# Kernel tuning notes

Hardware: AMD Instinct MI355X
Metric: run time of the kernel (lower is better)

The kernel has to match this reference:

```python
import jax, jax.numpy as jnp
import numpy as np

N = 80000
E = 1280000
EPS = 1e-5

def _lrelu(x):
    return jax.nn.leaky_relu(x, 0.01)

def _bn(h):
    # training-mode BatchNorm1d with batch size 1: stats over the node dim; affine is identity at init
    return (h - h.mean(0)) / jnp.sqrt(h.var(0) + EPS)

def _ln(h, g, b):
    m = h.mean(-1, keepdims=True)
    v = h.var(-1, keepdims=True)
    return (h - m) / jnp.sqrt(v + EPS) * g + b

def _gcn(h, w, b, src, dst, n):
    # PyG GCNConv: add self loops, symmetric deg^-1/2 normalization, aggregate at target
    hw = h @ w.T
    loop = jnp.arange(n, dtype=src.dtype)
    s = jnp.concatenate([src, loop])
    d = jnp.concatenate([dst, loop])
    deg = jax.ops.segment_sum(jnp.ones(d.shape, hw.dtype), d, num_segments=n)
    dinv = jnp.where(deg > 0, 1.0 / jnp.sqrt(deg), 0.0)
    msg = hw[s] * (dinv[s] * dinv[d])[:, None]  # [E+N, C]
    return jax.ops.segment_sum(msg, d, num_segments=n) + b

def _tnet(x, c1w, c1b, c2w, c2b, c3w, c3b, f1w, f1b, f2w, f2b, f3w, f3b):
    h = jax.nn.relu(x @ c1w.T + c1b)          # [N,64]  (source skips bn1)
    h = jax.nn.relu(_bn(h @ c2w.T + c2b))     # [N,128]
    h = jax.nn.relu(_bn(h @ c3w.T + c3b))     # [N,1024]
    g = h.max(0)                              # global max pool -> [1024]
    g = jax.nn.relu(g @ f1w.T + f1b)
    g = jax.nn.relu(g @ f2w.T + f2b)
    iden = jnp.array([1.0, 0.0, 0.0, 0.0, 1.0, 0.0, 0.0, 0.0, 1.0], x.dtype)
    g = g @ f3w.T + f3b + iden
    return g.reshape(3, 3)

def _forward(edge_index, x, tnet_c1_w, tnet_c1_b, tnet_c2_w, tnet_c2_b, tnet_c3_w, tnet_c3_b, tnet_fc1_w, tnet_fc1_b, tnet_fc2_w, tnet_fc2_b, tnet_fc3_w, tnet_fc3_b, conv1_w, conv1_b, g1_li_w, g1_li_b, g1_gcn_w, g1_gcn_b, g1_ln_g, g1_ln_b, conv2_w, conv2_b, g2_li_w, g2_li_b, g2_gcn_w, g2_gcn_b, g2_ln_g, g2_ln_b, conv3_w, conv3_b, out_w, out_b):
    src, dst = edge_index[0], edge_index[1]
    n = x.shape[0]
    T = _tnet(x, tnet_c1_w, tnet_c1_b, tnet_c2_w, tnet_c2_b, tnet_c3_w, tnet_c3_b, tnet_fc1_w, tnet_fc1_b, tnet_fc2_w, tnet_fc2_b, tnet_fc3_w, tnet_fc3_b)
    h0 = x @ T                                  # [N,3] spatial transform
    xg = _lrelu(h0 @ conv1_w.T + conv1_b)       # [N,64] (conv1d k=1 == per-node linear)
    # Gcn_Attention 1
    nf = _lrelu(xg @ g1_li_w.T + g1_li_b)
    nf2 = _lrelu(_gcn(nf, g1_gcn_w, g1_gcn_b, src, dst, n))
    h = _ln(jnp.concatenate([nf, nf2], 1), g1_ln_g, g1_ln_b)   # [N,128]
    h = _lrelu(h @ conv2_w.T + conv2_b)
    # Gcn_Attention 2
    nf = _lrelu(h @ g2_li_w.T + g2_li_b)
    nf2 = _lrelu(_gcn(nf, g2_gcn_w, g2_gcn_b, src, dst, n))
    h = _ln(jnp.concatenate([nf, nf2], 1), g2_ln_g, g2_ln_b)   # [N,256]
    h = jnp.concatenate([h, xg], 1)                            # [N,320]
    h = _lrelu(h @ conv3_w.T + conv3_b)                        # [N,256]
    pooled = h.mean(0)                                         # global mean pool (single graph)
    feat = jnp.concatenate([jnp.broadcast_to(pooled, (n, pooled.shape[0])), xg], 1)  # [N,320]
    return feat @ out_w.T + out_b                              # [N,4]

def setup_inputs():
    ki = iter(jax.random.split(jax.random.key(0), 32))
    def W(shape):
        return jax.random.normal(next(ki), shape, jnp.float32) * (1.0 / float(np.sqrt(shape[-1])))
    z = lambda n: jnp.zeros((n,), jnp.float32)
    o = lambda n: jnp.ones((n,), jnp.float32)
    inp = {}
    inp['x'] = jax.random.normal(next(ki), (N, 3), jnp.float32)
    inp['edge_index'] = jax.random.randint(next(ki), (2, E), 0, N, dtype=jnp.int32)
    inp['tnet_c1_w'] = W((64, 3)); inp['tnet_c1_b'] = z(64)
    inp['tnet_c2_w'] = W((128, 64)); inp['tnet_c2_b'] = z(128)
    inp['tnet_c3_w'] = W((1024, 128)); inp['tnet_c3_b'] = z(1024)
    inp['tnet_fc1_w'] = W((512, 1024)); inp['tnet_fc1_b'] = z(512)
    inp['tnet_fc2_w'] = W((256, 512)); inp['tnet_fc2_b'] = z(256)
    inp['tnet_fc3_w'] = W((9, 256)); inp['tnet_fc3_b'] = z(9)
    inp['conv1_w'] = W((64, 3)); inp['conv1_b'] = z(64)
    inp['g1_li_w'] = W((64, 64)); inp['g1_li_b'] = z(64)
    inp['g1_gcn_w'] = W((64, 64)); inp['g1_gcn_b'] = z(64)
    inp['g1_ln_g'] = o(128); inp['g1_ln_b'] = z(128)
    inp['conv2_w'] = W((128, 128)); inp['conv2_b'] = z(128)
    inp['g2_li_w'] = W((128, 128)); inp['g2_li_b'] = z(128)
    inp['g2_gcn_w'] = W((128, 128)); inp['g2_gcn_b'] = z(128)
    inp['g2_ln_g'] = o(256); inp['g2_ln_b'] = z(256)
    inp['conv3_w'] = W((256, 320)); inp['conv3_b'] = z(256)
    inp['out_w'] = W((4, 320)); inp['out_b'] = z(4)
    return inp

def reference(x, edge_index, tnet_c1_w, tnet_c1_b, tnet_c2_w, tnet_c2_b, tnet_c3_w, tnet_c3_b, tnet_fc1_w, tnet_fc1_b, tnet_fc2_w, tnet_fc2_b, tnet_fc3_w, tnet_fc3_b, conv1_w, conv1_b, g1_li_w, g1_li_b, g1_gcn_w, g1_gcn_b, g1_ln_g, g1_ln_b, conv2_w, conv2_b, g2_li_w, g2_li_b, g2_gcn_w, g2_gcn_b, g2_ln_g, g2_ln_b, conv3_w, conv3_b, out_w, out_b):
    return _forward(edge_index, x, tnet_c1_w, tnet_c1_b, tnet_c2_w, tnet_c2_b, tnet_c3_w, tnet_c3_b, tnet_fc1_w, tnet_fc1_b, tnet_fc2_w, tnet_fc2_b, tnet_fc3_w, tnet_fc3_b, conv1_w, conv1_b, g1_li_w, g1_li_b, g1_gcn_w, g1_gcn_b, g1_ln_g, g1_ln_b, conv2_w, conv2_b, g2_li_w, g2_li_b, g2_gcn_w, g2_gcn_b, g2_ln_g, g2_ln_b, conv3_w, conv3_b, out_w, out_b)
```

## Files before the change

### kernel.cpp

```cpp
#include <hip/hip_runtime.h>
#include <cstddef>

#define EPSV 1e-5f

typedef __attribute__((ext_vector_type(8))) short frag8;
typedef __attribute__((ext_vector_type(4))) float f32x4;

__device__ __forceinline__ float lrelu01(float v) { return v > 0.f ? v : 0.01f * v; }
__device__ __forceinline__ void atomAddF(float* p, float v) { unsafeAtomicAdd(p, v); }
__device__ __forceinline__ unsigned fkey(float f) {
    unsigned u = __float_as_uint(f);
    return (u & 0x80000000u) ? ~u : (u | 0x80000000u);
}
__device__ __forceinline__ unsigned short f2b(float f) {
    unsigned u = __float_as_uint(f);
    unsigned r = u + 0x7fffu + ((u >> 16) & 1u);
    return (unsigned short)(r >> 16);
}
__device__ __forceinline__ float b2f(unsigned short h) {
    return __uint_as_float(((unsigned)h) << 16);
}
__device__ __forceinline__ float blo(unsigned u) { return __uint_as_float(u << 16); }
__device__ __forceinline__ float bhi(unsigned u) { return __uint_as_float(u & 0xffff0000u); }

static inline unsigned cdivu(unsigned a, unsigned b) { return (a + b - 1) / b; }

__device__ __forceinline__ void gbar(unsigned* cnt, unsigned target) {
    __syncthreads();
    if (threadIdx.x == 0) {
        __threadfence();
        atomicAdd(cnt, 1u);
        while (atomicAdd(cnt, 0u) < target) { }
        __threadfence();
    }
    __syncthreads();
}


__device__ void degrank_body(int bid, const int* __restrict__ dst, int* __restrict__ deg,
                             int* __restrict__ rank, int E) {
    int e = bid * 256 + threadIdx.x;
    if (e < E) rank[e] = atomicAdd(&deg[dst[e]], 1);
}

__device__ void scan_local_body(int bid, const int* __restrict__ deg, int* __restrict__ startv,
                                int* __restrict__ bsum, float* __restrict__ dinv, int n) {
    __shared__ int t0[256];
    int tid = threadIdx.x;
    int i = bid * 256 + tid;
    int v = (i < n) ? deg[i] : 0;
    if (i < n) dinv[i] = rsqrtf((float)(v + 1));
    t0[tid] = v;
    __syncthreads();
    for (int o = 1; o < 256; o <<= 1) {
        int add = (tid >= o) ? t0[tid - o] : 0;
        __syncthreads();
        t0[tid] += add;
        __syncthreads();
    }
    if (i < n) startv[i] = t0[tid] - v;
    if (tid == 255) bsum[bid] = t0[255];
}

__device__ void scan_bsum_body(int* __restrict__ bsum, int nb) {
    __shared__ int t0[512];
    __shared__ int t1[512];
    int tid = threadIdx.x;
    int v0 = (tid < nb) ? bsum[tid] : 0;
    int v1 = (tid + 256 < nb) ? bsum[tid + 256] : 0;
    t0[tid] = v0; t0[tid + 256] = v1;
    __syncthreads();
    int* a = t0; int* b = t1;
    for (int o = 1; o < 512; o <<= 1) {
        b[tid]       = a[tid]       + ((tid >= o)       ? a[tid - o]       : 0);
        b[tid + 256] = a[tid + 256] + ((tid + 256 >= o) ? a[tid + 256 - o] : 0);
        __syncthreads();
        int* t = a; a = b; b = t;
    }
    if (tid < nb) bsum[tid] = a[tid] - v0;
    if (tid + 256 < nb) bsum[tid + 256] = a[tid + 256] - v1;
}

__device__ void fill_body(int bid, const int* __restrict__ src, const int* __restrict__ dst,
                          const int* __restrict__ rank, const int* __restrict__ startv,
                          const int* __restrict__ bsum, int* __restrict__ csr, int E) {
    int e = bid * 256 + threadIdx.x;
    if (e < E) {
        int d = dst[e];
        csr[startv[d] + bsum[d >> 8] + rank[e]] = src[e];
    }
}


__device__ void wconv_body(int bid, const float* __restrict__ s0, const float* __restrict__ s1,
                           const float* __restrict__ s2, const float* __restrict__ s3,
                           const float* __restrict__ s4, const float* __restrict__ s5,
                           const float* __restrict__ s6, const float* __restrict__ s7,
                           unsigned short* __restrict__ dst) {
    int t = bid * 256 + threadIdx.x;
    if (t >= 278528) return;
    const float* srcs[8] = {s0, s1, s2, s3, s4, s5, s6, s7};
    const int off[9] = {0, 8192, 139264, 143360, 147456, 163840, 180224, 196608, 278528};
    int seg = 0;
    while (t >= off[seg + 1]) ++seg;
    unsigned short v = f2b(srcs[seg][t - off[seg]]);
    if (seg == 1) {
        int li = t - 8192;
        int rch = li >> 7, k = li & 127;
        int cb = rch >> 7, r = rch & 127;
        int flat = ((r >> 4) * 4 + (k >> 5)) * 64 + ((k >> 3) & 3) * 16 + (r & 15);
        dst[8192 + cb * 16384 + flat * 8 + (k & 7)] = v;
    } else {
        dst[t] = v;
    }
}

__device__ void h1_body(int bid, const float* __restrict__ x, const float* __restrict__ w,
                        const float* __restrict__ b, unsigned short* __restrict__ h1, int n) {
    int node = bid * 256 + threadIdx.x;
    if (node >= n) return;
    float x0 = x[node * 3], x1 = x[node * 3 + 1], x2 = x[node * 3 + 2];
    unsigned short* o = h1 + (size_t)node * 64;
#pragma unroll
    for (int cp = 0; cp < 8; ++cp) {
        unsigned short tmp[8];
#pragma unroll
        for (int t = 0; t < 8; ++t) {
            int c = cp * 8 + t;
            float v = x0 * w[c * 3] + x1 * w[c * 3 + 1] + x2 * w[c * 3 + 2] + b[c];
            tmp[t] = f2b(fmaxf(v, 0.f));
        }
        *(float4*)(o + cp * 8) = *(float4*)tmp;
    }
}

__device__ void prebn_body(int bid, const float* __restrict__ z, const float* __restrict__ sum2,
                           const float* __restrict__ ss2, unsigned short* __restrict__ a3f,
                           int n16, float invn) {
    int t = bid * 256 + threadIdx.x;
    if (t >= n16) return;
    int row = t >> 4, cp = t & 15;
    int c = cp * 8;
    const float* src = z + (size_t)row * 128 + c;
    float4 v0 = *(const float4*)src;
    float4 v1 = *(const float4*)(src + 4);
    float vv[8] = {v0.x, v0.y, v0.z, v0.w, v1.x, v1.y, v1.z, v1.w};
    unsigned short o[8];
#pragma unroll
    for (int i = 0; i < 8; ++i) {
        float m = sum2[c + i] * invn;
        float var = ss2[c + i] * invn - m * m;
        o[i] = f2b(fmaxf((vv[i] - m) * rsqrtf(var + EPSV), 0.f));
    }
    int tile = row >> 7, r = row & 127;
    int flat = ((r >> 4) * 4 + (cp >> 2)) * 64 + (cp & 3) * 16 + (r & 15);
    *(float4*)(a3f + (size_t)tile * 16384 + flat * 8) = *(float4*)o;
}

enum { MF_BIAS = 1, MF_LRELU = 2, MF_DINV = 4, MF_STOREF = 8, MF_STOREB = 16,
       MF_STATS = 32, MF_COLSUM = 64 };

template <int BN, int MODE>
__device__ void mgemm_body(int bx, int by,
                           const unsigned short* __restrict__ A, int lda, int K,
                           const unsigned short* __restrict__ W,
                           const float* __restrict__ bias,
                           float* __restrict__ OutF, unsigned short* __restrict__ OutB, int ldo,
                           const float* __restrict__ dinv,
                           float* __restrict__ sum_o, float* __restrict__ ss_o,
                           unsigned* __restrict__ maxk_o) {
    constexpr int BM = 128;
    constexpr int LDT = 40;
    __shared__ unsigned short As[BM * LDT];
    __shared__ unsigned short Ws[BN * LDT];
    __shared__ float redS[2 * 128];
    __shared__ unsigned redM[128];

    const int tid = threadIdx.x;
    const int wid = tid >> 6, lane = tid & 63;
    const int quad = lane >> 4, lrow = lane & 15;
    const int bn0 = bx * BM;
    const int bc0 = by * BN;

    constexpr int NI = (BN == 128) ? 4 : 2;
    constexpr int NJ = 4;
    const int wm = (BN == 128) ? (wid & 1) * 64 : wid * 32;
    const int wn = (BN == 128) ? (wid >> 1) * 64 : 0;

    if (MODE & (MF_STATS | MF_COLSUM)) {
        for (int c = tid; c < BN; c += 256) {
            redS[c] = 0.f; redS[128 + c] = 0.f; redM[c] = 0u;
        }
    }

    f32x4 acc[NI][NJ] = {};

    for (int k0 = 0; k0 < K; k0 += 32) {
#pragma unroll
        for (int h = 0; h < 2; ++h) {
            int ch = tid + h * 256;
            int row = ch >> 2, cp = ch & 3;
            const unsigned short* src = A + (size_t)(bn0 + row) * lda + k0 + cp * 8;
            *(float4*)&As[row * LDT + cp * 8] = *(const float4*)src;
        }
#pragma unroll
        for (int h = 0; h < BN / 64; ++h) {
            int ch = tid + h * 256;
            int row = ch >> 2, cp = ch & 3;
            const unsigned short* src = W + (size_t)(bc0 + row) * K + k0 + cp * 8;
            *(float4*)&Ws[row * LDT + cp * 8] = *(const float4*)src;
        }
        __syncthreads();
        frag8 af[NI], bf[NJ];
#pragma unroll
        for (int i = 0; i < NI; ++i)
            af[i] = *(const frag8*)&As[(wm + i * 16 + lrow) * LDT + quad * 8];
#pragma unroll
        for (int j = 0; j < NJ; ++j)
            bf[j] = *(const frag8*)&Ws[(wn + j * 16 + lrow) * LDT + quad * 8];
#pragma unroll
        for (int i = 0; i < NI; ++i)
#pragma unroll
            for (int j = 0; j < NJ; ++j)
                acc[i][j] = __builtin_amdgcn_mfma_f32_16x16x32_bf16(af[i], bf[j], acc[i][j], 0, 0, 0);
        __syncthreads();
    }

#pragma unroll
    for (int j = 0; j < NJ; ++j) {
        const int col = bc0 + wn + j * 16 + lrow;
        float bv = (MODE & MF_BIAS) ? bias[col] : 0.f;
        float s = 0.f, q = 0.f, m = -3.4e38f;
#pragma unroll
        for (int i = 0; i < NI; ++i) {
            const int rowb = bn0 + wm + i * 16 + quad * 4;
#pragma unroll
            for (int r = 0; r < 4; ++r) {
                float t = acc[i][j][r] + bv;
                if (MODE & MF_LRELU) t = lrelu01(t);
                if (MODE & MF_DINV) t *= dinv[rowb + r];
                if (MODE & MF_STOREF) OutF[(size_t)(rowb + r) * ldo + col] = t;
                if (MODE & MF_STOREB) OutB[(size_t)(rowb + r) * ldo + col] = f2b(t);
                s += t; q += t * t; m = fmaxf(m, t);
            }
        }
        if (MODE & (MF_STATS | MF_COLSUM)) {
            s += __shfl_xor(s, 16); s += __shfl_xor(s, 32);
            if (MODE & MF_STATS) {
                q += __shfl_xor(q, 16); q += __shfl_xor(q, 32);
                m = fmaxf(m, __shfl_xor(m, 16)); m = fmaxf(m, __shfl_xor(m, 32));
            }
            if (quad == 0) {
                int lc = wn + j * 16 + lrow;
                atomicAdd(&redS[lc], s);
                if (MODE & MF_STATS) {
                    atomicAdd(&redS[128 + lc], q);
                    atomicMax(&redM[lc], fkey(m));
                }
            }
        }
    }
    if (MODE & (MF_STATS | MF_COLSUM)) {
        __syncthreads();
        for (int c = tid; c < BN; c += 256) {
            atomAddF(&sum_o[bc0 + c], redS[c]);
            if (MODE & MF_STATS) {
                atomAddF(&ss_o[bc0 + c], redS[128 + c]);
                atomicMax(&maxk_o[bc0 + c], redM[c]);
            }
        }
    }
}

template <int BN, int MODE, int SWAP>
__launch_bounds__(256)
__global__ void k_mgemm(const unsigned short* __restrict__ A, int lda, int K,
                        const unsigned short* __restrict__ W,
                        const float* __restrict__ bias,
                        float* __restrict__ OutF, unsigned short* __restrict__ OutB, int ldo,
                        const float* __restrict__ dinv,
                        float* __restrict__ sum_o, float* __restrict__ ss_o,
                        unsigned* __restrict__ maxk_o) {
    int bx = SWAP ? blockIdx.y : blockIdx.x;
    int by = SWAP ? blockIdx.x : blockIdx.y;
    mgemm_body<BN, MODE>(bx, by, A, lda, K, W, bias, OutF, OutB, ldo, dinv, sum_o, ss_o, maxk_o);
}

__device__ void z3_body(int bid,
                        const unsigned short* __restrict__ AF,
                        const unsigned short* __restrict__ WF,
                        const float* __restrict__ bias,
                        float* __restrict__ sum_o, float* __restrict__ ss_o,
                        unsigned* __restrict__ maxk_o, int ntiles) {
    const int tid = threadIdx.x;
    const int wid = tid >> 6, lane = tid & 63;
    const int quad = lane >> 4, lrow = lane & 15;

    int w = (bid & 7) * ntiles + (bid >> 3);
    const int tile = w >> 3;
    const int cb = w & 7;
    const unsigned short* At = AF + (size_t)tile * 16384;
    const unsigned short* Wt = WF + (size_t)cb * 16384;

    const int ar = (wid & 1) * 4;
    const int wc = (wid >> 1) * 4;
    f32x4 acc[4][4] = {};
#pragma unroll
    for (int kc = 0; kc < 4; ++kc) {
        frag8 af[4], bf[4];
#pragma unroll
        for (int i = 0; i < 4; ++i)
            af[i] = *(const frag8*)&At[(((ar + i) * 4 + kc) * 64 + lane) * 8];
#pragma unroll
        for (int j = 0; j < 4; ++j)
            bf[j] = *(const frag8*)&Wt[(((wc + j) * 4 + kc) * 64 + lane) * 8];
#pragma unroll
        for (int i = 0; i < 4; ++i)
#pragma unroll
            for (int j = 0; j < 4; ++j)
                acc[i][j] = __builtin_amdgcn_mfma_f32_16x16x32_bf16(af[i], bf[j], acc[i][j], 0, 0, 0);
    }

#pragma unroll
    for (int j = 0; j < 4; ++j) {
        int c = cb * 128 + (wc + j) * 16 + lrow;
        float bv = bias[c];
        float s = 0.f, q = 0.f, m = -3.4e38f;
#pragma unroll
        for (int i = 0; i < 4; ++i)
#pragma unroll
            for (int r = 0; r < 4; ++r) {
                float t = acc[i][j][r] + bv;
                s += t; q += t * t; m = fmaxf(m, t);
            }
        s += __shfl_xor(s, 16); s += __shfl_xor(s, 32);
        q += __shfl_xor(q, 16); q += __shfl_xor(q, 32);
        m = fmaxf(m, __shfl_xor(m, 16)); m = fmaxf(m, __shfl_xor(m, 32));
        if (quad == 0) {
            atomAddF(&sum_o[c], s);
            atomAddF(&ss_o[c], q);
            atomicMax(&maxk_o[c], fkey(m));
        }
    }
}


__launch_bounds__(256)
__global__ void FK1(const int* __restrict__ dst, int* __restrict__ deg, int* __restrict__ rank,
                    int E, int EB,
                    const float* s0, const float* s1, const float* s2, const float* s3,
                    const float* s4, const float* s5, const float* s6, const float* s7,
                    unsigned short* __restrict__ WB, int WCB,
                    const float* __restrict__ x, const float* __restrict__ c1w,
                    const float* __restrict__ c1b, unsigned short* __restrict__ B1, int n) {
    int b = blockIdx.x;
    if (b < EB) { degrank_body(b, dst, deg, rank, E); return; }
    b -= EB;
    if (b < WCB) { wconv_body(b, s0, s1, s2, s3, s4, s5, s6, s7, WB); return; }
    b -= WCB;
    h1_body(b, x, c1w, c1b, B1, n);
}

__launch_bounds__(256)
__global__ void FK2(const unsigned short* __restrict__ A, int lda, int K,
                    const unsigned short* __restrict__ W, const float* __restrict__ bias,
                    float* __restrict__ OutF, int ldo,
                    float* __restrict__ sum_o, float* __restrict__ ss_o,
                    unsigned* __restrict__ maxk_o, int GXz,
                    const int* __restrict__ deg, int* __restrict__ startv,
                    int* __restrict__ bsum, float* __restrict__ dinvv, int n) {
    if ((int)blockIdx.x < GXz)
        mgemm_body<128, (MF_BIAS | MF_STOREF | MF_STATS)>(
            blockIdx.x, 0, A, lda, K, W, bias, OutF, nullptr, ldo, nullptr, sum_o, ss_o, maxk_o);
    else
        scan_local_body(blockIdx.x - GXz, deg, startv, bsum, dinvv, n);
}

__launch_bounds__(256)
__global__ void FK3(const float* __restrict__ z, const float* __restrict__ sum2,
                    const float* __restrict__ ss2, unsigned short* __restrict__ a3f,
                    int n16, float invn, int PB, int* __restrict__ bsum, int nb) {
    if ((int)blockIdx.x < PB) prebn_body(blockIdx.x, z, sum2, ss2, a3f, n16, invn);
    else scan_bsum_body(bsum, nb);
}

__launch_bounds__(256)
__global__ void FK4(const unsigned short* __restrict__ AF, const unsigned short* __restrict__ WF,
                    const float* __restrict__ bias,
                    float* __restrict__ sum_o, float* __restrict__ ss_o,
                    unsigned* __restrict__ maxk_o, int ntiles, int NZ,
                    const int* __restrict__ src, const int* __restrict__ dst,
                    const int* __restrict__ rank, const int* __restrict__ startv,
                    const int* __restrict__ bsum, int* __restrict__ csr, int E) {
    if ((int)blockIdx.x < NZ) z3_body(blockIdx.x, AF, WF, bias, sum_o, ss_o, maxk_o, ntiles);
    else fill_body(blockIdx.x - NZ, src, dst, rank, startv, bsum, csr, E);
}

__launch_bounds__(256)
__global__ void k_tnet(const float* __restrict__ sum3, const float* __restrict__ ss3,
                       const unsigned* __restrict__ maxk,
                       const float* __restrict__ f1w, const float* __restrict__ f1b,
                       const float* __restrict__ f2w, const float* __restrict__ f2bias,
                       const float* __restrict__ f3w, const float* __restrict__ f3b,
                       float* __restrict__ a1, float* __restrict__ a2,
                       float* __restrict__ T9,
                       unsigned* __restrict__ cnt1, unsigned* __restrict__ cnt2, float invn) {
    __shared__ float g[1024];
    __shared__ float a1s[512];
    int tid = threadIdx.x;
    int bid = blockIdx.x;
    for (int c = tid; c < 1024; c += 256) {
        float m = sum3[c] * invn;
        float var = ss3[c] * invn - m * m;
        unsigned k = maxk[c];
        unsigned u = (k & 0x80000000u) ? (k & 0x7FFFFFFFu) : ~k;
        g[c] = fmaxf((__uint_as_float(u) - m) * rsqrtf(var + EPSV), 0.f);
    }
    __syncthreads();
    {
        int row = bid * 64 + (tid >> 2);
        int part = tid & 3;
        const float* w = f1w + (size_t)row * 1024 + part * 256;
        const float* gg = g + part * 256;
        float s = 0.f;
#pragma unroll 4
        for (int k = 0; k < 256; k += 4) {
            float4 wv = *(const float4*)(w + k);
            s = fmaf(wv.x, gg[k], s);
            s = fmaf(wv.y, gg[k + 1], s);
            s = fmaf(wv.z, gg[k + 2], s);
            s = fmaf(wv.w, gg[k + 3], s);
        }
        s += __shfl_xor(s, 1); s += __shfl_xor(s, 2);
        if (part == 0) a1[row] = fmaxf(s + f1b[row], 0.f);
    }
    gbar(cnt1, 8);
    a1s[tid] = a1[tid];
    a1s[tid + 256] = a1[tid + 256];
    __syncthreads();
    {
        int row = bid * 32 + (tid >> 3);
        int part = tid & 7;
        const float* w = f2w + (size_t)row * 512 + part * 64;
        const float* aa = a1s + part * 64;
        float s = 0.f;
#pragma unroll 4
        for (int k = 0; k < 64; k += 4) {
            float4 wv = *(const float4*)(w + k);
            s = fmaf(wv.x, aa[k], s);
            s = fmaf(wv.y, aa[k + 1], s);
            s = fmaf(wv.z, aa[k + 2], s);
            s = fmaf(wv.w, aa[k + 3], s);
        }
        s += __shfl_xor(s, 1); s += __shfl_xor(s, 2); s += __shfl_xor(s, 4);
        if (part == 0) a2[row] = fmaxf(s + f2bias[row], 0.f);
    }
    gbar(cnt2, 8);
    if (bid == 0 && tid < 144) {
        int r = tid >> 4, kk = (tid & 15) * 16;
        const float* wr = f3w + r * 256 + kk;
        float s = 0.f;
#pragma unroll
        for (int k = 0; k < 16; ++k) s = fmaf(wr[k], a2[kk + k], s);
        s += __shfl_xor(s, 1); s += __shfl_xor(s, 2);
        s += __shfl_xor(s, 4); s += __shfl_xor(s, 8);
        if ((tid & 15) == 0) {
            s += f3b[r];
            if (r == 0 || r == 4 || r == 8) s += 1.f;
            T9[r] = s;
        }
    }
}

template <int CH>
__launch_bounds__(256)
__global__ void k_gln(const int* __restrict__ startv, const int* __restrict__ bsum,
                      const int* __restrict__ degv,
                      const int* __restrict__ csr, const unsigned short* __restrict__ q,
                      const unsigned short* __restrict__ nf, const float* __restrict__ dinv,
                      const float* __restrict__ gcn_b, const float* __restrict__ lng,
                      const float* __restrict__ lnb, unsigned short* __restrict__ outp,
                      int ldo, int n) {
    constexpr int GRP = (CH == 64) ? 8 : 4;
    constexpr int PL  = 64 / GRP;
    constexpr int TT  = 16 / GRP;
    constexpr int CPL = CH / PL;
    const int wv = threadIdx.x >> 6, lane = threadIdx.x & 63;
    const int g = lane / PL, p = lane & (PL - 1);
    int node = blockIdx.x * 4 + wv;
    if (node >= n) return;

    const unsigned short* qp = q + (size_t)p * CPL;

    float acc[CPL];
    {
        uint4 v = *(const uint4*)(qp + (size_t)node * CH);
        unsigned sv[4] = {v.x, v.y, v.z, v.w};
        if (g == 0) {
#pragma unroll
            for (int d = 0; d < 4; ++d) { acc[2 * d] = blo(sv[d]); acc[2 * d + 1] = bhi(sv[d]); }
        } else {
#pragma unroll
            for (int k = 0; k < CPL; ++k) acc[k] = 0.f;
        }
    }

    int s0 = startv[node] + bsum[node >> 8], cnt = degv[node];
    const int* cs = csr + s0;
    int sidx[TT];
#pragma unroll
    for (int t = 0; t < TT; ++t) { int j = t * GRP + g; sidx[t] = (j < cnt) ? cs[j] : n; }
    for (int j0 = 0; j0 < cnt; j0 += 16) {
        uint4 buf[TT];
#pragma unroll
        for (int t = 0; t < TT; ++t)
            buf[t] = *(const uint4*)(qp + (size_t)(unsigned)sidx[t] * CH);
#pragma unroll
        for (int t = 0; t < TT; ++t) {
            int j = j0 + 16 + t * GRP + g;
            sidx[t] = (j < cnt) ? cs[j] : n;
        }
#pragma unroll
        for (int t = 0; t < TT; ++t) {
            unsigned bw[4] = {buf[t].x, buf[t].y, buf[t].z, buf[t].w};
#pragma unroll
            for (int d = 0; d < 4; ++d) {
                acc[2 * d] += blo(bw[d]);
                acc[2 * d + 1] += bhi(bw[d]);
            }
        }
    }

#pragma unroll
    for (int k = 0; k < CPL; ++k) {
#pragma unroll
        for (int off = PL; off < 64; off <<= 1) acc[k] += __shfl_xor(acc[k], off);
    }

    float di = dinv[node];
    float nv[CPL], bv[CPL];
    {
        uint4 v = *(const uint4*)(nf + (size_t)node * CH + p * CPL);
        unsigned sv[4] = {v.x, v.y, v.z, v.w};
#pragma unroll
        for (int d = 0; d < 4; ++d) { nv[2 * d] = blo(sv[d]); nv[2 * d + 1] = bhi(sv[d]); }
    }
    const float* gb = gcn_b + p * CPL;
#pragma unroll
    for (int k = 0; k < CPL; ++k) bv[k] = lrelu01(di * acc[k] + gb[k]);

    float s = 0.f, ss = 0.f;
#pragma unroll
    for (int k = 0; k < CPL; ++k) { s += nv[k] + bv[k]; ss += nv[k] * nv[k] + bv[k] * bv[k]; }
#pragma unroll
    for (int off = 32; off > 0; off >>= 1) { s += __shfl_xor(s, off); ss += __shfl_xor(ss, off); }
    const float inv = 1.f / (float)(GRP * 2 * CH);
    float mu = s * inv;
    float var = ss * inv - mu * mu;
    float rsg = rsqrtf(var + EPSV);

    unsigned short* orow = outp + (size_t)node * ldo;
    if (g == 0) {
        unsigned short tmp[CPL];
        const float* lg = lng + p * CPL; const float* lb = lnb + p * CPL;
#pragma unroll
        for (int k = 0; k < CPL; ++k) tmp[k] = f2b((nv[k] - mu) * rsg * lg[k] + lb[k]);
        *(uint4*)(orow + p * CPL) = *(uint4*)tmp;
    } else if (g == 1) {
        unsigned short tmp[CPL];
        const float* lg = lng + CH + p * CPL; const float* lb = lnb + CH + p * CPL;
#pragma unroll
        for (int k = 0; k < CPL; ++k) tmp[k] = f2b((bv[k] - mu) * rsg * lg[k] + lb[k]);
        *(uint4*)(orow + CH + p * CPL) = *(uint4*)tmp;
    }
}


__launch_bounds__(256)
__global__ void k_xg2(const float* __restrict__ x, const float* __restrict__ T9,
                      const float* __restrict__ w, const float* __restrict__ b,
                      const float* __restrict__ ow,
                      unsigned short* __restrict__ xg, float* __restrict__ xdot, int n) {
    __shared__ float owS[256];
    __shared__ float T9s[9];
    int tid = threadIdx.x;
    owS[tid] = ow[(tid >> 6) * 320 + 256 + (tid & 63)];
    if (tid < 9) T9s[tid] = T9[tid];
    __syncthreads();
    int node = blockIdx.x * 256 + tid;
    if (node >= n) return;
    float x0 = x[node * 3], x1 = x[node * 3 + 1], x2 = x[node * 3 + 2];
    float h0 = x0 * T9s[0] + x1 * T9s[3] + x2 * T9s[6];
    float h1 = x0 * T9s[1] + x1 * T9s[4] + x2 * T9s[7];
    float h2 = x0 * T9s[2] + x1 * T9s[5] + x2 * T9s[8];
    unsigned short* o = xg + (size_t)node * 320;
    float d0 = 0.f, d1 = 0.f, d2 = 0.f, d3 = 0.f;
#pragma unroll
    for (int cp = 0; cp < 8; ++cp) {
        unsigned short tmp[8];
#pragma unroll
        for (int t = 0; t < 8; ++t) {
            int c = cp * 8 + t;
            float v = lrelu01(h0 * w[c * 3] + h1 * w[c * 3 + 1] + h2 * w[c * 3 + 2] + b[c]);
            tmp[t] = f2b(v);
            d0 = fmaf(v, owS[c], d0);
            d1 = fmaf(v, owS[64 + c], d1);
            d2 = fmaf(v, owS[128 + c], d2);
            d3 = fmaf(v, owS[192 + c], d3);
        }
        *(float4*)(o + cp * 8) = *(float4*)tmp;
    }
    *(float4*)(xdot + (size_t)node * 4) = make_float4(d0, d1, d2, d3);
}

template <int BN>
__launch_bounds__(256)
__global__ void k_ligc(const unsigned short* __restrict__ A, int lda, int K,
                       const unsigned short* __restrict__ Wli, const float* __restrict__ bli,
                       const unsigned short* __restrict__ Wgc, const float* __restrict__ dinv,
                       unsigned short* __restrict__ NF, int ldnf,
                       unsigned short* __restrict__ Q, int ldq) {
    constexpr int BM = 128;
    constexpr int LDT = 40;
    constexpr int LDT2 = BN + 8;
    __shared__ unsigned short SA[BM * LDT2];
    __shared__ unsigned short Ws[BN * LDT];

    const int tid = threadIdx.x;
    const int wid = tid >> 6, lane = tid & 63;
    const int quad = lane >> 4, lrow = lane & 15;
    const int bn0 = blockIdx.x * BM;
    constexpr int NI = (BN == 128) ? 4 : 2;
    constexpr int NJ = 4;
    const int wm = (BN == 128) ? (wid & 1) * 64 : wid * 32;
    const int wn = (BN == 128) ? (wid >> 1) * 64 : 0;

    {
        f32x4 acc[NI][NJ] = {};
        for (int k0 = 0; k0 < K; k0 += 32) {
#pragma unroll
            for (int h = 0; h < 2; ++h) {
                int ch = tid + h * 256;
                int row = ch >> 2, cp = ch & 3;
                *(float4*)&SA[row * LDT + cp * 8] =
                    *(const float4*)(A + (size_t)(bn0 + row) * lda + k0 + cp * 8);
            }
#pragma unroll
            for (int h = 0; h < BN / 64; ++h) {
                int ch = tid + h * 256;
                int row = ch >> 2, cp = ch & 3;
                *(float4*)&Ws[row * LDT + cp * 8] =
                    *(const float4*)(Wli + (size_t)row * K + k0 + cp * 8);
            }
            __syncthreads();
            frag8 af[NI], bf[NJ];
#pragma unroll
            for (int i = 0; i < NI; ++i)
                af[i] = *(const frag8*)&SA[(wm + i * 16 + lrow) * LDT + quad * 8];
#pragma unroll
            for (int j = 0; j < NJ; ++j)
                bf[j] = *(const frag8*)&Ws[(wn + j * 16 + lrow) * LDT + quad * 8];
#pragma unroll
            for (int i = 0; i < NI; ++i)
#pragma unroll
                for (int j = 0; j < NJ; ++j)
                    acc[i][j] = __builtin_amdgcn_mfma_f32_16x16x32_bf16(af[i], bf[j], acc[i][j], 0, 0, 0);
            __syncthreads();
        }
#pragma unroll
        for (int j = 0; j < NJ; ++j) {
            const int col = wn + j * 16 + lrow;
            float bv = bli[col];
#pragma unroll
            for (int i = 0; i < NI; ++i) {
                const int rowl = wm + i * 16 + quad * 4;
#pragma unroll
                for (int r = 0; r < 4; ++r) {
                    unsigned short h = f2b(lrelu01(acc[i][j][r] + bv));
                    NF[(size_t)(bn0 + rowl + r) * ldnf + col] = h;
                    SA[(rowl + r) * LDT2 + col] = h;
                }
            }
        }
        __syncthreads();
    }
    {
        f32x4 acc[NI][NJ] = {};
        for (int k0 = 0; k0 < BN; k0 += 32) {
#pragma unroll
            for (int h = 0; h < BN / 64; ++h) {
                int ch = tid + h * 256;
                int row = ch >> 2, cp = ch & 3;
                *(float4*)&Ws[row * LDT + cp * 8] =
                    *(const float4*)(Wgc + (size_t)row * BN + k0 + cp * 8);
            }
            __syncthreads();
            frag8 af[NI], bf[NJ];
#pragma unroll
            for (int i = 0; i < NI; ++i)
                af[i] = *(const frag8*)&SA[(wm + i * 16 + lrow) * LDT2 + k0 + quad * 8];
#pragma unroll
            for (int j = 0; j < NJ; ++j)
                bf[j] = *(const frag8*)&Ws[(wn + j * 16 + lrow) * LDT + quad * 8];
#pragma unroll
            for (int i = 0; i < NI; ++i)
#pragma unroll
                for (int j = 0; j < NJ; ++j)
                    acc[i][j] = __builtin_amdgcn_mfma_f32_16x16x32_bf16(af[i], bf[j], acc[i][j], 0, 0, 0);
            __syncthreads();
        }
#pragma unroll
        for (int j = 0; j < NJ; ++j) {
            const int col = wn + j * 16 + lrow;
#pragma unroll
            for (int i = 0; i < NI; ++i) {
                const int rowb = bn0 + wm + i * 16 + quad * 4;
#pragma unroll
                for (int r = 0; r < 4; ++r) {
                    float t = acc[i][j][r] * dinv[rowb + r];
                    Q[(size_t)(rowb + r) * ldq + col] = f2b(t);
                }
            }
        }
    }
}

__global__ void k_out2(const float* __restrict__ xdot, const float* __restrict__ ow,
                       const float* __restrict__ ob, const float* __restrict__ pooled,
                       float* __restrict__ out, int n, float invn) {
    __shared__ float c4s[4];
    int tid = threadIdx.x;
    {
        int j = tid >> 6, lane = tid & 63;
        float s = 0.f;
        for (int c = lane; c < 256; c += 64) s += pooled[c] * invn * ow[j * 320 + c];
#pragma unroll
        for (int off = 32; off > 0; off >>= 1) s += __shfl_down(s, off);
        if (lane == 0) c4s[j] = s + ob[j];
    }
    __syncthreads();
    int node = blockIdx.x * 256 + tid;
    if (node >= n) return;
    float4 xd = *(const float4*)(xdot + (size_t)node * 4);
    *(float4*)(out + (size_t)node * 4) =
        make_float4(c4s[0] + xd.x, c4s[1] + xd.y, c4s[2] + xd.z, c4s[3] + xd.w);
}


extern "C" void kernel_launch(void* const* d_in, const int* in_sizes, int n_in,
                              void* d_out, int out_size, void* d_ws, size_t ws_size,
                              hipStream_t stream) {
    const float* x   = (const float*)d_in[0];
    const int*   ei  = (const int*)d_in[1];
    const float* c1w = (const float*)d_in[2];  const float* c1b = (const float*)d_in[3];
    const float* c2w = (const float*)d_in[4];  const float* c2b = (const float*)d_in[5];
    const float* c3w = (const float*)d_in[6];  const float* c3b = (const float*)d_in[7];
    const float* f1w = (const float*)d_in[8];  const float* f1b = (const float*)d_in[9];
    const float* f2w = (const float*)d_in[10]; const float* f2bp = (const float*)d_in[11];
    const float* f3w = (const float*)d_in[12]; const float* f3b = (const float*)d_in[13];
    const float* cv1w = (const float*)d_in[14]; const float* cv1b = (const float*)d_in[15];
    const float* li1w = (const float*)d_in[16]; const float* li1b = (const float*)d_in[17];
    const float* gc1w = (const float*)d_in[18]; const float* gc1b = (const float*)d_in[19];
    const float* ln1g = (const float*)d_in[20]; const float* ln1b = (const float*)d_in[21];
    const float* cv2w = (const float*)d_in[22]; const float* cv2b = (const float*)d_in[23];
    const float* li2w = (const float*)d_in[24]; const float* li2b = (const float*)d_in[25];
    const float* gc2w = (const float*)d_in[26]; const float* gc2b = (const float*)d_in[27];
    const float* ln2g = (const float*)d_in[28]; const float* ln2b = (const float*)d_in[29];
    const float* cv3w = (const float*)d_in[30]; const float* cv3b = (const float*)d_in[31];
    const float* ow  = (const float*)d_in[32]; const float* ob  = (const float*)d_in[33];
    float* out = (float*)d_out;

    const int N = in_sizes[0] / 3;
    const int E = in_sizes[1] / 2;
    const int* srcI = ei;
    const int* dstI = ei + E;

    char* base = (char*)d_ws;
    size_t off = 0;
    auto take = [&](size_t bytes) -> char* {
        char* p = base + off;
        off = (off + bytes + 255) & ~(size_t)255;
        return p;
    };
    int*   deg    = (int*)  take((size_t)N * 4);
    float* dinv   = (float*)take((size_t)N * 4);
    int*   startv = (int*)  take((size_t)N * 4);
    int*   rank   = (int*)  take((size_t)E * 4);
    int*   csr    = (int*)  take((size_t)E * 4);
    int*   bsum   = (int*)  take(512 * 4);
    float* sm     = (float*)take(8192 * 4);
    unsigned short* WB = (unsigned short*)take(278528 * 2);
    unsigned short* H  = (unsigned short*)take((size_t)N * 320 * 2);
    float* F1 = (float*)take((size_t)N * 128 * 4);
    unsigned short* B1 = (unsigned short*)take((size_t)N * 64 * 2);
    unsigned short* B2 = (unsigned short*)take(((size_t)N * 128 + 128) * 2);
    unsigned short* B3 = (unsigned short*)take((size_t)N * 128 * 2);
    float* XD = (float*)take((size_t)N * 4 * 4);

    unsigned short* c2wb  = WB + 0;
    unsigned short* c3wf  = WB + 8192;
    unsigned short* li1wb = WB + 139264;
    unsigned short* gc1wb = WB + 143360;
    unsigned short* cv2wb = WB + 147456;
    unsigned short* li2wb = WB + 163840;
    unsigned short* gc2wb = WB + 180224;
    unsigned short* cv3wb = WB + 196608;

    float* sum2 = sm + 0;    float* ss2 = sm + 128;
    float* sum3 = sm + 256;  float* ss3 = sm + 1280;
    unsigned* maxk = (unsigned*)(sm + 2304);
    float* pooled = sm + 3328;
    unsigned* dmax = (unsigned*)(sm + 3584);
    unsigned* cnt1 = (unsigned*)(sm + 3712);
    unsigned* cnt2 = (unsigned*)(sm + 3713);
    float* T9  = sm + 3968;
    float* a1  = sm + 5120;
    float* a2  = sm + 5760;

    const float invn = 1.0f / (float)N;
    const dim3 blk(256);
    const unsigned GX = (unsigned)(N / 128);
    const unsigned NB = cdivu((unsigned)N, 256);
    const unsigned EB = cdivu((unsigned)E, 256);
    const unsigned WCB = cdivu(278528u, 256);
    const unsigned PB = cdivu((unsigned)N * 16, 256);

    hipMemsetAsync(deg, 0, (size_t)N * 4, stream);
    hipMemsetAsync(sm, 0, 3720 * 4, stream);
    hipMemsetAsync(B2 + (size_t)N * 128, 0, 256, stream);

    FK1<<<EB + WCB + NB, blk, 0, stream>>>(dstI, deg, rank, E, (int)EB,
                                           c2w, c3w, li1w, gc1w, cv2w, li2w, gc2w, cv3w,
                                           WB, (int)WCB, x, c1w, c1b, B1, N);
    FK2<<<GX + NB, blk, 0, stream>>>(B1, 64, 64, c2wb, c2b, F1, 128,
                                     sum2, ss2, dmax, (int)GX, deg, startv, bsum, dinv, N);
    FK3<<<PB + 1, blk, 0, stream>>>(F1, sum2, ss2, B2, N * 16, invn, (int)PB, bsum, (int)NB);
    FK4<<<8 * GX + EB, blk, 0, stream>>>(B2, c3wf, c3b, sum3, ss3, maxk, (int)GX,
                                         (int)(8 * GX), srcI, dstI, rank, startv, bsum, csr, E);
    hipMemsetAsync(B2 + (size_t)N * 64, 0, 128, stream);
    k_tnet<<<8, blk, 0, stream>>>(sum3, ss3, maxk, f1w, f1b, f2w, f2bp, f3w, f3b,
                                  a1, a2, T9, cnt1, cnt2, invn);
    k_xg2<<<NB, blk, 0, stream>>>(x, T9, cv1w, cv1b, ow, H + 256, XD, N);

    k_ligc<64><<<GX, blk, 0, stream>>>(H + 256, 320, 64, li1wb, li1b, gc1wb, dinv, B1, 64, B2, 64);
    k_gln<64><<<cdivu((unsigned)N, 4), blk, 0, stream>>>(
        startv, bsum, deg, csr, B2, B1, dinv, gc1b, ln1g, ln1b, B3, 128, N);
    k_mgemm<128, (MF_BIAS | MF_LRELU | MF_STOREB), 0><<<dim3(GX, 1), blk, 0, stream>>>(
        B3, 128, 128, cv2wb, cv2b, nullptr, B2, 128, nullptr, nullptr, nullptr, nullptr);

    k_ligc<128><<<GX, blk, 0, stream>>>(B2, 128, 128, li2wb, li2b, gc2wb, dinv, B3, 128, B2, 128);
    k_gln<128><<<cdivu((unsigned)N, 4), blk, 0, stream>>>(
        startv, bsum, deg, csr, B2, B3, dinv, gc2b, ln2g, ln2b, H, 320, N);

    k_mgemm<128, (MF_BIAS | MF_LRELU | MF_COLSUM), 1><<<dim3(2, GX), blk, 0, stream>>>(
        H, 320, 320, cv3wb, cv3b, nullptr, nullptr, 0, nullptr, pooled, nullptr, nullptr);

    k_out2<<<NB, blk, 0, stream>>>(XD, ow, ob, pooled, out, N, invn);
}
```

Baseline: 504.4 us.

## Fuse conv2 with second li/gcn GEMMs, interleave FK4 blocks, widen tnet FC

Measured after the change: 630.8 us. 1.25x slower.

```diff
diff --git a/kernel.cpp b/kernel.cpp
--- a/kernel.cpp
+++ b/kernel.cpp
@@ -291,14 +291,13 @@
                         const unsigned short* __restrict__ WF,
                         const float* __restrict__ bias,
                         float* __restrict__ sum_o, float* __restrict__ ss_o,
-                        unsigned* __restrict__ maxk_o, int ntiles) {
+                        unsigned* __restrict__ maxk_o) {
     const int tid = threadIdx.x;
     const int wid = tid >> 6, lane = tid & 63;
     const int quad = lane >> 4, lrow = lane & 15;
 
-    int w = (bid & 7) * ntiles + (bid >> 3);
-    const int tile = w >> 3;
-    const int cb = w & 7;
+    const int tile = bid >> 3;
+    const int cb = bid & 7;
     const unsigned short* At = AF + (size_t)tile * 16384;
     const unsigned short* Wt = WF + (size_t)cb * 16384;
 
@@ -388,12 +387,20 @@
 __global__ void FK4(const unsigned short* __restrict__ AF, const unsigned short* __restrict__ WF,
                     const float* __restrict__ bias,
                     float* __restrict__ sum_o, float* __restrict__ ss_o,
-                    unsigned* __restrict__ maxk_o, int ntiles, int NZ,
+                    unsigned* __restrict__ maxk_o, int NZ, int EB,
                     const int* __restrict__ src, const int* __restrict__ dst,
                     const int* __restrict__ rank, const int* __restrict__ startv,
                     const int* __restrict__ bsum, int* __restrict__ csr, int E) {
-    if ((int)blockIdx.x < NZ) z3_body(blockIdx.x, AF, WF, bias, sum_o, ss_o, maxk_o, ntiles);
-    else fill_body(blockIdx.x - NZ, src, dst, rank, startv, bsum, csr, E);
+    int b = blockIdx.x;
+    int mn = (NZ < EB) ? NZ : EB;
+    if (b < 2 * mn) {
+        if ((b & 1) == 0) z3_body(b >> 1, AF, WF, bias, sum_o, ss_o, maxk_o);
+        else fill_body(b >> 1, src, dst, rank, startv, bsum, csr, E);
+    } else if (NZ > EB) {
+        z3_body(b - EB, AF, WF, bias, sum_o, ss_o, maxk_o);
+    } else {
+        fill_body(b - NZ, src, dst, rank, startv, bsum, csr, E);
+    }
 }
 
 __launch_bounds__(256)
@@ -418,13 +425,13 @@
     }
     __syncthreads();
     {
-        int row = bid * 64 + (tid >> 2);
-        int part = tid & 3;
-        const float* w = f1w + (size_t)row * 1024 + part * 256;
-        const float* gg = g + part * 256;
+        int row = bid * 16 + (tid >> 4);
+        int part = tid & 15;
+        const float* w = f1w + (size_t)row * 1024 + part * 64;
+        const float* gg = g + part * 64;
         float s = 0.f;
 #pragma unroll 4
-        for (int k = 0; k < 256; k += 4) {
+        for (int k = 0; k < 64; k += 4) {
             float4 wv = *(const float4*)(w + k);
             s = fmaf(wv.x, gg[k], s);
             s = fmaf(wv.y, gg[k + 1], s);
@@ -432,20 +439,21 @@
             s = fmaf(wv.w, gg[k + 3], s);
         }
         s += __shfl_xor(s, 1); s += __shfl_xor(s, 2);
+        s += __shfl_xor(s, 4); s += __shfl_xor(s, 8);
         if (part == 0) a1[row] = fmaxf(s + f1b[row], 0.f);
     }
-    gbar(cnt1, 8);
+    gbar(cnt1, 32);
     a1s[tid] = a1[tid];
     a1s[tid + 256] = a1[tid + 256];
     __syncthreads();
     {
-        int row = bid * 32 + (tid >> 3);
-        int part = tid & 7;
-        const float* w = f2w + (size_t)row * 512 + part * 64;
-        const float* aa = a1s + part * 64;
+        int row = bid * 8 + (tid >> 5);
+        int part = tid & 31;
+        const float* w = f2w + (size_t)row * 512 + part * 16;
+        const float* aa = a1s + part * 16;
         float s = 0.f;
-#pragma unroll 4
-        for (int k = 0; k < 64; k += 4) {
+#pragma unroll
+        for (int k = 0; k < 16; k += 4) {
             float4 wv = *(const float4*)(w + k);
             s = fmaf(wv.x, aa[k], s);
             s = fmaf(wv.y, aa[k + 1], s);
@@ -453,9 +461,10 @@
             s = fmaf(wv.w, aa[k + 3], s);
         }
         s += __shfl_xor(s, 1); s += __shfl_xor(s, 2); s += __shfl_xor(s, 4);
+        s += __shfl_xor(s, 8); s += __shfl_xor(s, 16);
         if (part == 0) a2[row] = fmaxf(s + f2bias[row], 0.f);
     }
-    gbar(cnt2, 8);
+    gbar(cnt2, 32);
     if (bid == 0 && tid < 144) {
         int r = tid >> 4, kk = (tid & 15) * 16;
         const float* wr = f3w + r * 256 + kk;
@@ -480,7 +489,7 @@
                       const unsigned short* __restrict__ nf, const float* __restrict__ dinv,
                       const float* __restrict__ gcn_b, const float* __restrict__ lng,
                       const float* __restrict__ lnb, unsigned short* __restrict__ outp,
-                      int ldo, int n) {
+                      int ldo, int n, int nd) {
     constexpr int GRP = (CH == 64) ? 8 : 4;
     constexpr int PL  = 64 / GRP;
     constexpr int TT  = 16 / GRP;
@@ -509,7 +518,7 @@
     const int* cs = csr + s0;
     int sidx[TT];
 #pragma unroll
-    for (int t = 0; t < TT; ++t) { int j = t * GRP + g; sidx[t] = (j < cnt) ? cs[j] : n; }
+    for (int t = 0; t < TT; ++t) { int j = t * GRP + g; sidx[t] = (j < cnt) ? cs[j] : nd; }
     for (int j0 = 0; j0 < cnt; j0 += 16) {
         uint4 buf[TT];
 #pragma unroll
@@ -518,7 +527,7 @@
 #pragma unroll
         for (int t = 0; t < TT; ++t) {
             int j = j0 + 16 + t * GRP + g;
-            sidx[t] = (j < cnt) ? cs[j] : n;
+            sidx[t] = (j < cnt) ? cs[j] : nd;
         }
 #pragma unroll
         for (int t = 0; t < TT; ++t) {
@@ -625,6 +634,7 @@
     constexpr int LDT2 = BN + 8;
     __shared__ unsigned short SA[BM * LDT2];
     __shared__ unsigned short Ws[BN * LDT];
+    __shared__ unsigned short As[BM * LDT];
 
     const int tid = threadIdx.x;
     const int wid = tid >> 6, lane = tid & 63;
@@ -642,7 +652,7 @@
             for (int h = 0; h < 2; ++h) {
                 int ch = tid + h * 256;
                 int row = ch >> 2, cp = ch & 3;
-                *(float4*)&SA[row * LDT + cp * 8] =
+                *(float4*)&As[row * LDT + cp * 8] =
                     *(const float4*)(A + (size_t)(bn0 + row) * lda + k0 + cp * 8);
             }
 #pragma unroll
@@ -656,7 +666,7 @@
             frag8 af[NI], bf[NJ];
 #pragma unroll
             for (int i = 0; i < NI; ++i)
-                af[i] = *(const frag8*)&SA[(wm + i * 16 + lrow) * LDT + quad * 8];
+                af[i] = *(const frag8*)&As[(wm + i * 16 + lrow) * LDT + quad * 8];
 #pragma unroll
             for (int j = 0; j < NJ; ++j)
                 bf[j] = *(const frag8*)&Ws[(wn + j * 16 + lrow) * LDT + quad * 8];
@@ -720,6 +730,148 @@
                     float t = acc[i][j][r] * dinv[rowb + r];
                     Q[(size_t)(rowb + r) * ldq + col] = f2b(t);
                 }
+            }
+        }
+    }
+}
+
+__launch_bounds__(256)
+__global__ void k_cligc(const unsigned short* __restrict__ A,
+                        const unsigned short* __restrict__ Wcv, const float* __restrict__ bcv,
+                        const unsigned short* __restrict__ Wli, const float* __restrict__ bli,
+                        const unsigned short* __restrict__ Wgc, const float* __restrict__ dinv,
+                        unsigned short* __restrict__ NF,
+                        unsigned short* __restrict__ Q) {
+    constexpr int LDT = 40;
+    constexpr int LDT2 = 136;
+    __shared__ unsigned short As[128 * LDT];
+    __shared__ unsigned short Ws[128 * LDT];
+    __shared__ unsigned short SA[128 * LDT2];
+
+    const int tid = threadIdx.x;
+    const int wid = tid >> 6, lane = tid & 63;
+    const int quad = lane >> 4, lrow = lane & 15;
+    const int bn0 = blockIdx.x * 128;
+    const int wm = (wid & 1) * 64;
+    const int wn = (wid >> 1) * 64;
+
+    {
+        f32x4 acc[4][4] = {};
+        for (int k0 = 0; k0 < 128; k0 += 32) {
+#pragma unroll
+            for (int h = 0; h < 2; ++h) {
+                int ch = tid + h * 256;
+                int row = ch >> 2, cp = ch & 3;
+                *(float4*)&As[row * LDT + cp * 8] =
+                    *(const float4*)(A + (size_t)(bn0 + row) * 128 + k0 + cp * 8);
+                *(float4*)&Ws[row * LDT + cp * 8] =
+                    *(const float4*)(Wcv + (size_t)row * 128 + k0 + cp * 8);
+            }
+            __syncthreads();
+            frag8 af[4], bf[4];
+#pragma unroll
+            for (int i = 0; i < 4; ++i)
+                af[i] = *(const frag8*)&As[(wm + i * 16 + lrow) * LDT + quad * 8];
+#pragma unroll
+            for (int j = 0; j < 4; ++j)
+                bf[j] = *(const frag8*)&Ws[(wn + j * 16 + lrow) * LDT + quad * 8];
+#pragma unroll
+            for (int i = 0; i < 4; ++i)
+#pragma unroll
+                for (int j = 0; j < 4; ++j)
+                    acc[i][j] = __builtin_amdgcn_mfma_f32_16x16x32_bf16(af[i], bf[j], acc[i][j], 0, 0, 0);
+            __syncthreads();
+        }
+#pragma unroll
+        for (int j = 0; j < 4; ++j) {
+            const int col = wn + j * 16 + lrow;
+            float bv = bcv[col];
+#pragma unroll
+            for (int i = 0; i < 4; ++i) {
+                const int rowl = wm + i * 16 + quad * 4;
+#pragma unroll
+                for (int r = 0; r < 4; ++r)
+                    SA[(rowl + r) * LDT2 + col] = f2b(lrelu01(acc[i][j][r] + bv));
+            }
+        }
+        __syncthreads();
+    }
+    {
+        f32x4 acc[4][4] = {};
+        for (int k0 = 0; k0 < 128; k0 += 32) {
+#pragma unroll
+            for (int h = 0; h < 2; ++h) {
+                int ch = tid + h * 256;
+                int row = ch >> 2, cp = ch & 3;
+                *(float4*)&Ws[row * LDT + cp * 8] =
+                    *(const float4*)(Wli + (size_t)row * 128 + k0 + cp * 8);
+            }
+            __syncthreads();
+            frag8 af[4], bf[4];
+#pragma unroll
+            for (int i = 0; i < 4; ++i)
+                af[i] = *(const frag8*)&SA[(wm + i * 16 + lrow) * LDT2 + k0 + quad * 8];
+#pragma unroll
+            for (int j = 0; j < 4; ++j)
+                bf[j] = *(const frag8*)&Ws[(wn + j * 16 + lrow) * LDT + quad * 8];
+#pragma unroll
+            for (int i = 0; i < 4; ++i)
+#pragma unroll
+                for (int j = 0; j < 4; ++j)
+                    acc[i][j] = __builtin_amdgcn_mfma_f32_16x16x32_bf16(af[i], bf[j], acc[i][j], 0, 0, 0);
+            __syncthreads();
+        }
+#pragma unroll
+        for (int j = 0; j < 4; ++j) {
+            const int col = wn + j * 16 + lrow;
+            float bv = bli[col];
+#pragma unroll
+            for (int i = 0; i < 4; ++i) {
+                const int rowl = wm + i * 16 + quad * 4;
+#pragma unroll
+                for (int r = 0; r < 4; ++r) {
+                    unsigned short h = f2b(lrelu01(acc[i][j][r] + bv));
+                    NF[(size_t)(bn0 + rowl + r) * 128 + col] = h;
+                    SA[(rowl + r) * LDT2 + col] = h;
+                }
+            }
+        }
+        __syncthreads();
+    }
+    {
+        f32x4 acc[4][4] = {};
+        for (int k0 = 0; k0 < 128; k0 += 32) {
+#pragma unroll
+            for (int h = 0; h < 2; ++h) {
+                int ch = tid + h * 256;
+                int row = ch >> 2, cp = ch & 3;
+                *(float4*)&Ws[row * LDT + cp * 8] =
+                    *(const float4*)(Wgc + (size_t)row * 128 + k0 + cp * 8);
+            }
+            __syncthreads();
+            frag8 af[4], bf[4];
+#pragma unroll
+            for (int i = 0; i < 4; ++i)
+                af[i] = *(const frag8*)&SA[(wm + i * 16 + lrow) * LDT2 + k0 + quad * 8];
+#pragma unroll
+            for (int j = 0; j < 4; ++j)
+                bf[j] = *(const frag8*)&Ws[(wn + j * 16 + lrow) * LDT + quad * 8];
+#pragma unroll
+            for (int i = 0; i < 4; ++i)
+#pragma unroll
+                for (int j = 0; j < 4; ++j)
+                    acc[i][j] = __builtin_amdgcn_mfma_f32_16x16x32_bf16(af[i], bf[j], acc[i][j], 0, 0, 0);
+            __syncthreads();
+        }
+#pragma unroll
+        for (int j = 0; j < 4; ++j) {
+            const int col = wn + j * 16 + lrow;
+#pragma unroll
+            for (int i = 0; i < 4; ++i) {
+                const int rowb = bn0 + wm + i * 16 + quad * 4;
+#pragma unroll
+                for (int r = 0; r < 4; ++r)
+                    Q[(size_t)(rowb + r) * 128 + col] = f2b(acc[i][j][r] * dinv[rowb + r]);
             }
         }
     }
@@ -783,12 +935,12 @@
         return p;
     };
     int*   deg    = (int*)  take((size_t)N * 4);
+    float* sm     = (float*)take(8192 * 4);
     float* dinv   = (float*)take((size_t)N * 4);
     int*   startv = (int*)  take((size_t)N * 4);
     int*   rank   = (int*)  take((size_t)E * 4);
     int*   csr    = (int*)  take((size_t)E * 4);
     int*   bsum   = (int*)  take(512 * 4);
-    float* sm     = (float*)take(8192 * 4);
     unsigned short* WB = (unsigned short*)take(278528 * 2);
     unsigned short* H  = (unsigned short*)take((size_t)N * 320 * 2);
     float* F1 = (float*)take((size_t)N * 128 * 4);
@@ -824,9 +976,10 @@
     const unsigned EB = cdivu((unsigned)E, 256);
     const unsigned WCB = cdivu(278528u, 256);
     const unsigned PB = cdivu((unsigned)N * 16, 256);
-
-    hipMemsetAsync(deg, 0, (size_t)N * 4, stream);
-    hipMemsetAsync(sm, 0, 3720 * 4, stream);
+    const unsigned NZ = 8 * GX;
+
+    size_t degpad = ((size_t)N * 4 + 255) & ~(size_t)255;
+    hipMemsetAsync(deg, 0, degpad + 3720 * 4, stream);
     hipMemsetAsync(B2 + (size_t)N * 128, 0, 256, stream);
 
     FK1<<<EB + WCB + NB, blk, 0, stream>>>(dstI, deg, rank, E, (int)EB,
@@ -835,22 +988,19 @@
     FK2<<<GX + NB, blk, 0, stream>>>(B1, 64, 64, c2wb, c2b, F1, 128,
                                      sum2, ss2, dmax, (int)GX, deg, startv, bsum, dinv, N);
     FK3<<<PB + 1, blk, 0, stream>>>(F1, sum2, ss2, B2, N * 16, invn, (int)PB, bsum, (int)NB);
-    FK4<<<8 * GX + EB, blk, 0, stream>>>(B2, c3wf, c3b, sum3, ss3, maxk, (int)GX,
-                                         (int)(8 * GX), srcI, dstI, rank, startv, bsum, csr, E);
-    hipMemsetAsync(B2 + (size_t)N * 64, 0, 128, stream);
-    k_tnet<<<8, blk, 0, stream>>>(sum3, ss3, maxk, f1w, f1b, f2w, f2bp, f3w, f3b,
-                                  a1, a2, T9, cnt1, cnt2, invn);
+    FK4<<<NZ + EB, blk, 0, stream>>>(B2, c3wf, c3b, sum3, ss3, maxk, (int)NZ, (int)EB,
+                                     srcI, dstI, rank, startv, bsum, csr, E);
+    k_tnet<<<32, blk, 0, stream>>>(sum3, ss3, maxk, f1w, f1b, f2w, f2bp, f3w, f3b,
+                                   a1, a2, T9, cnt1, cnt2, invn);
     k_xg2<<<NB, blk, 0, stream>>>(x, T9, cv1w, cv1b, ow, H + 256, XD, N);
 
     k_ligc<64><<<GX, blk, 0, stream>>>(H + 256, 320, 64, li1wb, li1b, gc1wb, dinv, B1, 64, B2, 64);
     k_gln<64><<<cdivu((unsigned)N, 4), blk, 0, stream>>>(
-        startv, bsum, deg, csr, B2, B1, dinv, gc1b, ln1g, ln1b, B3, 128, N);
-    k_mgemm<128, (MF_BIAS | MF_LRELU | MF_STOREB), 0><<<dim3(GX, 1), blk, 0, stream>>>(
-        B3, 128, 128, cv2wb, cv2b, nullptr, B2, 128, nullptr, nullptr, nullptr, nullptr);
-
-    k_ligc<128><<<GX, blk, 0, stream>>>(B2, 128, 128, li2wb, li2b, gc2wb, dinv, B3, 128, B2, 128);
+        startv, bsum, deg, csr, B2, B1, dinv, gc1b, ln1g, ln1b, B3, 128, N, 2 * N);
+
+    k_cligc<<<GX, blk, 0, stream>>>(B3, cv2wb, cv2b, li2wb, li2b, gc2wb, dinv, B3, B2);
     k_gln<128><<<cdivu((unsigned)N, 4), blk, 0, stream>>>(
-        startv, bsum, deg, csr, B2, B3, dinv, gc2b, ln2g, ln2b, H, 320, N);
+        startv, bsum, deg, csr, B2, B3, dinv, gc2b, ln2g, ln2b, H, 320, N, N);
 
     k_mgemm<128, (MF_BIAS | MF_LRELU | MF_COLSUM), 1><<<dim3(2, GX), blk, 0, stream>>>(
         H, 320, 320, cv3wb, cv3b, nullptr, nullptr, 0, nullptr, pooled, nullptr, nullptr);
```
